# Kernel optimization log

Measured on AMD Instinct MI355X. Metric: run time of the kernel, lower is better.

## Reference

```python
import math
import jax, jax.numpy as jnp
import numpy as np

B = 8192
BAND = 5      # channels per DGCN
N = 62        # graph nodes (EEG electrodes)
LAYERS = 2
CBAM_C = (LAYERS + 1) * BAND  # 15
RED = 4
H2 = 64
K_TOP = int(N * 0.8)  # 49


def conv1x1(x, w, b):
    # x: [B,C,N,T], w: [O,C], b: [O] or None
    y = jnp.einsum('bcnt,oc->bont', x, w)
    if b is not None:
        y = y + b[None, :, None, None]
    return y


def dgcn(x, conv_w, conv_b, mem, gfc_w, gfc_b, gcn_w, gcn_b):
    skip = x
    x = conv1x1(x, conv_w, conv_b)
    scale = 1.0 / math.sqrt(BAND)
    # dynamic adjacency 1: memory-based
    a1 = jax.nn.softmax(jax.nn.relu(jnp.einsum('bcnt,cm->bnm', x, mem) * scale), axis=-1)
    # dynamic adjacency 2: self-similarity of time-summed features
    xs = jnp.sum(x, axis=-1)  # [B,C,N]
    a2 = jax.nn.softmax(jax.nn.relu(jnp.einsum('bcn,bcm->bnm', xs, xs) * scale), axis=-1)
    af = jnp.stack([a1, a2], axis=-1)          # [B,N,N,2]
    af = jnp.einsum('bnmk,ok->bnmo', af, gfc_w)[..., 0] + gfc_b[0]  # fc(2->1), squeeze
    af = jax.nn.softmax(af, axis=-1)
    _, idx = jax.lax.top_k(af, K_TOP)          # [B,N,k]
    bI = jnp.arange(af.shape[0])[:, None, None]
    nI = jnp.arange(N)[None, :, None]
    mask = jnp.zeros_like(af).at[bI, nI, idx].set(1.0)
    adj = af * mask
    # diffusion step (diffusion_step=1)
    y = jnp.einsum('bcnt,bnm->bcmt', x, adj)
    y = conv1x1(y, gcn_w, gcn_b)
    return y + skip


def cbam(x, ca_w1, ca_w2, sa_w, sa_b):
    residual = x
    # channel attention: shared SE MLP on max- and avg-pooled descriptors
    mx = jnp.max(x, axis=(2, 3), keepdims=True)   # [B,C,1,1]
    av = jnp.mean(x, axis=(2, 3), keepdims=True)
    def se(z):
        z = jnp.einsum('bcnt,oc->bont', z, ca_w1)
        z = jax.nn.relu(z)
        return jnp.einsum('bcnt,oc->bont', z, ca_w2)
    ca = jax.nn.sigmoid(se(mx) + se(av))
    out = x * ca
    # spatial attention: 3x3 conv over [max,mean] channel maps
    smax = jnp.max(out, axis=1, keepdims=True)
    smean = jnp.mean(out, axis=1, keepdims=True)
    s = jnp.concatenate([smax, smean], axis=1)    # [B,2,H,W]
    sa = jax.lax.conv_general_dilated(
        s, sa_w, window_strides=(1, 1), padding=((1, 1), (1, 1)),
        dimension_numbers=('NCHW', 'OIHW', 'NCHW')) + sa_b[None, :, None, None]
    sa = jax.nn.sigmoid(sa)
    out = out * sa
    return out + residual


def setup_inputs() -> dict:
    key = jax.random.key(0)
    ks = jax.random.split(key, 24)
    p = {}
    p['x'] = jax.random.normal(ks[0], (B, BAND * N), dtype=jnp.float32)
    for l in range(LAYERS):
        o = 1 + l * 8
        p[f'l{l}_conv_w'] = jax.random.normal(ks[o + 0], (BAND, BAND), jnp.float32) * 0.3
        p[f'l{l}_conv_b'] = jnp.zeros((BAND,), jnp.float32)
        p[f'l{l}_mem'] = jax.random.normal(ks[o + 1], (BAND, N), jnp.float32) * 0.2
        p[f'l{l}_gfc_w'] = jax.random.normal(ks[o + 2], (1, 2), jnp.float32) * 0.5
        p[f'l{l}_gfc_b'] = jnp.zeros((1,), jnp.float32)
        p[f'l{l}_gcn_w'] = jax.random.normal(ks[o + 3], (BAND, BAND), jnp.float32) * 0.3
        p[f'l{l}_gcn_b'] = jnp.zeros((BAND,), jnp.float32)
    p['ca_w1'] = jax.random.normal(ks[17], (CBAM_C // RED, CBAM_C), jnp.float32) * 0.2
    p['ca_w2'] = jax.random.normal(ks[18], (CBAM_C, CBAM_C // RED), jnp.float32) * 0.2
    p['sa_w'] = jax.random.normal(ks[19], (1, 2, 3, 3), jnp.float32) * 0.2
    p['sa_b'] = jnp.zeros((1,), jnp.float32)
    p['fc1_w'] = jax.random.normal(ks[20], (H2, N * CBAM_C), jnp.float32) * 0.03
    p['fc1_b'] = jnp.zeros((H2,), jnp.float32)
    p['fc2_w'] = jax.random.normal(ks[21], (H2, H2), jnp.float32) * 0.1
    p['fc2_b'] = jnp.zeros((H2,), jnp.float32)
    return p


def reference(x,
              l0_conv_w, l0_conv_b, l0_mem, l0_gfc_w, l0_gfc_b, l0_gcn_w, l0_gcn_b,
              l1_conv_w, l1_conv_b, l1_mem, l1_gfc_w, l1_gfc_b, l1_gcn_w, l1_gcn_b,
              ca_w1, ca_w2, sa_w, sa_b, fc1_w, fc1_b, fc2_w, fc2_b):
    h = x.reshape(x.shape[0], BAND, N)[:, :, :, None]  # [B,5,62,1]
    feats = [h]
    layer_params = [
        (l0_conv_w, l0_conv_b, l0_mem, l0_gfc_w, l0_gfc_b, l0_gcn_w, l0_gcn_b),
        (l1_conv_w, l1_conv_b, l1_mem, l1_gfc_w, l1_gfc_b, l1_gcn_w, l1_gcn_b),
    ]
    cur = h
    for lp in layer_params:
        cur = dgcn(cur, *lp)
        feats.append(cur)
    g = jnp.concatenate(feats, axis=1)                 # [B,15,62,1]
    g = cbam(g, ca_w1, ca_w2, sa_w, sa_b)
    out = g.reshape(g.shape[0], -1)
    out = jax.nn.relu(out @ fc1_w.T + fc1_b)           # dropout = identity (eval)
    out = jax.nn.relu(out @ fc2_w.T + fc2_b)
    return out
```

## Files before the change

### kernel.cpp

```cpp
#include <hip/hip_runtime.h>

#define NB 62
#define NC 5
#define KTOP 49

typedef unsigned short ushort_t;
typedef unsigned int uint_t;

__device__ __forceinline__ float sigmf(float x) {
    return 1.0f / (1.0f + __expf(-x));
}

__device__ __forceinline__ ushort_t f2b(float f) {
    union { float f; uint_t u; } cv; cv.f = f;
    uint_t r = (cv.u + 0x7fffu + ((cv.u >> 16) & 1u)) >> 16;
    return (ushort_t)r;
}
__device__ __forceinline__ float b2f(ushort_t h) {
    union { uint_t u; float f; } cv; cv.u = ((uint_t)h) << 16;
    return cv.f;
}
__device__ __forceinline__ float blo(uint_t w) {
    union { uint_t u; float f; } cv; cv.u = w << 16; return cv.f;
}
__device__ __forceinline__ float bhi(uint_t w) {
    union { uint_t u; float f; } cv; cv.u = w & 0xffff0000u; return cv.f;
}

__device__ __forceinline__ float tmax62(const float* a) {
    float t0 = a[0], t1 = a[1], t2 = a[2], t3 = a[3];
    #pragma unroll
    for (int m = 4; m < 60; m += 4) {
        t0 = fmaxf(t0, a[m]);     t1 = fmaxf(t1, a[m + 1]);
        t2 = fmaxf(t2, a[m + 2]); t3 = fmaxf(t3, a[m + 3]);
    }
    t0 = fmaxf(t0, a[60]); t1 = fmaxf(t1, a[61]);
    return fmaxf(fmaxf(t0, t1), fmaxf(t2, t3));
}
__device__ __forceinline__ float tsum62(const float* a) {
    float t0 = a[0], t1 = a[1], t2 = a[2], t3 = a[3];
    #pragma unroll
    for (int m = 4; m < 60; m += 4) {
        t0 += a[m]; t1 += a[m + 1]; t2 += a[m + 2]; t3 += a[m + 3];
    }
    t0 += a[60]; t1 += a[61];
    return (t0 + t1) + (t2 + t3);
}

__global__ void repack_kernel(const float* __restrict__ fc1w,
                              const float* __restrict__ fc2w,
                              ushort_t* __restrict__ w1o,
                              float* __restrict__ w2o) {
    const int i = blockIdx.x * 256 + threadIdx.x;
    if (i < 117 * 64 * 8) {
        const int j = i & 7, o = (i >> 3) & 63, i8 = i >> 9;
        const int src = i8 * 8 + j;
        const float v = (src < 930) ? fc1w[o * 930 + src] : 0.0f;
        w1o[i] = f2b(v);
    } else if (i < 117 * 64 * 8 + 16 * 64 * 4) {
        const int i2 = i - 117 * 64 * 8;
        const int j = i2 & 3, o = (i2 >> 2) & 63, k4 = i2 >> 8;
        w2o[i2] = fc2w[o * 64 + k4 * 4 + j];
    }
}

template <int L>
__device__ __forceinline__ void dgcn_layer(
    const int tid, const float* __restrict__ xin_g,
    const float* __restrict__ conv_w, const float* __restrict__ conv_b,
    const float* __restrict__ memp,
    const float* __restrict__ gfc_w, const float* __restrict__ gfc_b,
    const float* __restrict__ gcn_w, const float* __restrict__ gcn_b,
    float (*__restrict__ s_xc4)[4], float (*__restrict__ s_me4)[4],
    float (*__restrict__ s_t45)[2], ushort_t* __restrict__ s_adjh,
    float (*__restrict__ s_x1)[NC], float* __restrict__ f2out)
{
    const float scale = 0.44721359549995793f;

    for (int i = tid; i < NC * NB; i += 64) {
        const int c = i / NB, m = i - c * NB;
        if (c < 4) s_me4[m][c] = memp[i];
        else       s_t45[m][1] = memp[i];
    }

    float cw[25], cbv[5];
    #pragma unroll
    for (int i = 0; i < 25; ++i) cw[i] = conv_w[i];
    #pragma unroll
    for (int i = 0; i < 5; ++i)  cbv[i] = conv_b[i];
    const float w0 = gfc_w[0], w1 = gfc_w[1], b0 = gfc_b[0];

    float xo0 = 0, xo1 = 0, xo2 = 0, xo3 = 0, xo4 = 0;
    if (tid < NB) {
        float xn[5];
        #pragma unroll
        for (int c = 0; c < 5; ++c)
            xn[c] = (L == 0) ? xin_g[c * NB + tid] : s_x1[tid][c];
        xo0 = cbv[0]; xo1 = cbv[1]; xo2 = cbv[2]; xo3 = cbv[3]; xo4 = cbv[4];
        #pragma unroll
        for (int c = 0; c < 5; ++c) {
            xo0 = fmaf(cw[c],      xn[c], xo0);
            xo1 = fmaf(cw[5 + c],  xn[c], xo1);
            xo2 = fmaf(cw[10 + c], xn[c], xo2);
            xo3 = fmaf(cw[15 + c], xn[c], xo3);
            xo4 = fmaf(cw[20 + c], xn[c], xo4);
        }
        s_xc4[tid][0] = xo0; s_xc4[tid][1] = xo1;
        s_xc4[tid][2] = xo2; s_xc4[tid][3] = xo3;
        s_t45[tid][0] = xo4;
    }
    __syncthreads();

    if (tid < NB) {
        float r1[NB];
        float r2[64];
        #pragma unroll
        for (int m = 0; m < NB; ++m) {
            const float4 xc03 = *(const float4*)&s_xc4[m][0];
            const float4 me03 = *(const float4*)&s_me4[m][0];
            const float2 t45  = *(const float2*)&s_t45[m][0];
            float s1 = xo0 * me03.x + xo1 * me03.y + xo2 * me03.z + xo3 * me03.w + xo4 * t45.y;
            float s2 = xo0 * xc03.x + xo1 * xc03.y + xo2 * xc03.z + xo3 * xc03.w + xo4 * t45.x;
            r1[m] = fmaxf(s1 * scale, 0.0f);
            r2[m] = fmaxf(s2 * scale, 0.0f);
        }
        const float mx1 = tmax62(r1);
        #pragma unroll
        for (int m = 0; m < NB; ++m) r1[m] = __expf(r1[m] - mx1);
        const float inv1 = 1.0f / tsum62(r1);
        const float mx2 = tmax62(r2);
        #pragma unroll
        for (int m = 0; m < NB; ++m) r2[m] = __expf(r2[m] - mx2);
        const float inv2 = 1.0f / tsum62(r2);
        #pragma unroll
        for (int m = 0; m < NB; ++m)
            r1[m] = b0 + (r1[m] * inv1) * w0 + (r2[m] * inv2) * w1;
        const float mxa = tmax62(r1);
        #pragma unroll
        for (int m = 0; m < NB; ++m) r1[m] = __expf(r1[m] - mxa);
        const float inva = 1.0f / tsum62(r1);
        #pragma unroll
        for (int m = 0; m < NB; ++m) r1[m] *= inva;

        #pragma unroll
        for (int m = 0; m < NB; ++m) r2[m] = r1[m];
        r2[62] = INFINITY; r2[63] = INFINITY;
        #pragma unroll
        for (int k = 2; k <= 64; k <<= 1) {
            #pragma unroll
            for (int j = k >> 1; j > 0; j >>= 1) {
                #pragma unroll
                for (int i = 0; i < 64; ++i) {
                    const int p = i ^ j;
                    if (p > i) {
                        const bool up = ((i & k) == 0);
                        const float a = r2[i], c = r2[p];
                        r2[i] = up ? fminf(a, c) : fmaxf(a, c);
                        r2[p] = up ? fmaxf(a, c) : fminf(a, c);
                    }
                }
            }
        }
        const float vth = r2[13];

        int gc0 = 0, gc1 = 0, gc2 = 0, gc3 = 0;
        #pragma unroll
        for (int m = 0; m < 60; m += 4) {
            gc0 += (r1[m] > vth);     gc1 += (r1[m + 1] > vth);
            gc2 += (r1[m + 2] > vth); gc3 += (r1[m + 3] > vth);
        }
        gc0 += (r1[60] > vth); gc1 += (r1[61] > vth);
        const int G = (gc0 + gc1) + (gc2 + gc3);
        int eq = 0;
        #pragma unroll
        for (int m = 0; m < NB; ++m) {
            const bool e  = (r1[m] == vth);
            const bool ss = (r1[m] > vth) || (e && (G + eq) < KTOP);
            s_adjh[tid * NB + m] = f2b(ss ? r1[m] : 0.0f);
            eq += e ? 1 : 0;
        }
    }
    __syncthreads();

    if (tid < NB) {
        const int m = tid;
        float y0 = 0, y1 = 0, y2 = 0, y3 = 0, y4 = 0;
        for (int n = 0; n < NB; ++n) {
            const float a = b2f(s_adjh[n * NB + m]);
            const float4 xv = *(const float4*)&s_xc4[n][0];
            const float  xv4 = s_t45[n][0];
            y0 = fmaf(xv.x, a, y0); y1 = fmaf(xv.y, a, y1); y2 = fmaf(xv.z, a, y2);
            y3 = fmaf(xv.w, a, y3); y4 = fmaf(xv4, a, y4);
        }
        float gwv[25], gbv[5];
        #pragma unroll
        for (int i = 0; i < 25; ++i) gwv[i] = gcn_w[i];
        #pragma unroll
        for (int i = 0; i < 5; ++i)  gbv[i] = gcn_b[i];
        #pragma unroll
        for (int o = 0; o < 5; ++o) {
            const float z = gbv[o] + gwv[o * 5 + 0] * y0 + gwv[o * 5 + 1] * y1 +
                            gwv[o * 5 + 2] * y2 + gwv[o * 5 + 3] * y3 + gwv[o * 5 + 4] * y4;
            const float fi = (L == 0) ? xin_g[o * NB + m] : s_x1[m][o];
            const float zz = z + fi;
            if (L == 0) s_x1[m][o] = zz;
            else        f2out[o]   = zz;
        }
    }
    __syncthreads();
}

__global__ void __launch_bounds__(64) __attribute__((amdgpu_waves_per_eu(2, 3)))
encoder_kernel(
    const float* __restrict__ g_x,
    const float* __restrict__ c0w, const float* __restrict__ c0b,
    const float* __restrict__ m0,  const float* __restrict__ f0w,
    const float* __restrict__ f0b, const float* __restrict__ g0w,
    const float* __restrict__ g0b,
    const float* __restrict__ c1w, const float* __restrict__ c1b,
    const float* __restrict__ m1,  const float* __restrict__ f1w,
    const float* __restrict__ f1b, const float* __restrict__ g1w,
    const float* __restrict__ g1b,
    const float* __restrict__ caw1, const float* __restrict__ caw2,
    const float* __restrict__ saw,  const float* __restrict__ sab,
    const float* __restrict__ fc1w, const float* __restrict__ fc1b,
    const float* __restrict__ fc2w, const float* __restrict__ fc2b,
    const ushort_t* __restrict__ w1b, const float* __restrict__ w2p,
    const int use_ws,
    float* __restrict__ g_out)
{
    const int b   = blockIdx.x;
    const int tid = threadIdx.x;

    __shared__ __align__(16) float s_xc4[NB][4];
    __shared__ __align__(16) float s_me4[NB][4];
    __shared__ __align__(16) float s_t45[NB][2];
    __shared__ __align__(16) ushort_t s_adjh[NB * NB];
    __shared__ __align__(16) float s_x1[NB][NC];

    float* const s_g  = (float*)s_adjh;
    float* const s_h1 = ((float*)s_adjh) + 936;

    const float* xin = g_x + (size_t)b * (NC * NB);

    float f2[5] = {0, 0, 0, 0, 0};
    dgcn_layer<0>(tid, xin, c0w, c0b, m0, f0w, f0b, g0w, g0b,
                  s_xc4, s_me4, s_t45, s_adjh, s_x1, nullptr);
    dgcn_layer<1>(tid, xin, c1w, c1b, m1, f1w, f1b, g1w, g1b,
                  s_xc4, s_me4, s_t45, s_adjh, s_x1, f2);

    float f0[5], f1v[5];
    #pragma unroll
    for (int c = 0; c < 5; ++c) {
        f0[c]  = (tid < NB) ? xin[c * NB + tid] : 0.0f;
        f1v[c] = (tid < NB) ? s_x1[tid][c] : 0.0f;
    }

    float mxp[15], avp[15];
    #pragma unroll
    for (int c = 0; c < 15; ++c) {
        const float v = (c < 5) ? f0[c] : (c < 10) ? f1v[c - 5] : f2[c - 10];
        float vm = (tid < NB) ? v : -INFINITY;
        float vs = (tid < NB) ? v : 0.0f;
        #pragma unroll
        for (int off = 32; off > 0; off >>= 1) {
            vm = fmaxf(vm, __shfl_xor(vm, off, 64));
            vs += __shfl_xor(vs, off, 64);
        }
        mxp[c] = vm;
        avp[c] = vs * (1.0f / 62.0f);
    }
    float ca[15];
    {
        float hm[3], ha[3];
        #pragma unroll
        for (int o = 0; o < 3; ++o) {
            float am = 0.0f, aa = 0.0f;
            #pragma unroll
            for (int c = 0; c < 15; ++c) {
                const float w = caw1[o * 15 + c];
                am = fmaf(mxp[c], w, am);
                aa = fmaf(avp[c], w, aa);
            }
            hm[o] = fmaxf(am, 0.0f);
            ha[o] = fmaxf(aa, 0.0f);
        }
        #pragma unroll
        for (int c = 0; c < 15; ++c) {
            float t = 0.0f;
            #pragma unroll
            for (int o = 0; o < 3; ++o) t = fmaf(hm[o] + ha[o], caw2[c * 3 + o], t);
            ca[c] = sigmf(t);
        }
    }
    float og[15];
    float smx = -INFINITY, ssum = 0.0f;
    #pragma unroll
    for (int c = 0; c < 15; ++c) {
        const float fv = (c < 5) ? f0[c] : (c < 10) ? f1v[c - 5] : f2[c - 10];
        const float v = fv * ca[c];
        og[c] = v;
        smx = fmaxf(smx, v);
        ssum += v;
    }
    const float smean = ssum * (1.0f / 15.0f);
    const float sxl = __shfl_up(smx, 1, 64),   sml = __shfl_up(smean, 1, 64);
    const float sxr = __shfl_down(smx, 1, 64), smr = __shfl_down(smean, 1, 64);
    const float mskL = (tid > 0) ? 1.0f : 0.0f;
    const float mskR = (tid < NB - 1) ? 1.0f : 0.0f;
    float t = sab[0];
    t += mskL * (sxl * saw[1] + sml * saw[10]);
    t += smx * saw[4] + smean * saw[13];
    t += mskR * (sxr * saw[7] + smr * saw[16]);
    const float sa = sigmf(t);

    __syncthreads();
    if (tid < NB) {
        #pragma unroll
        for (int c = 0; c < 15; ++c) {
            const float fv = (c < 5) ? f0[c] : (c < 10) ? f1v[c - 5] : f2[c - 10];
            s_g[c * NB + tid] = og[c] * sa + fv;
        }
    }
    if (tid < 6) s_g[930 + tid] = 0.0f;
    __syncthreads();

    if (use_ws) {
        float acc = fc1b[tid];
        const uint4* w1v = (const uint4*)w1b;
        #pragma unroll 4
        for (int i8 = 0; i8 < 117; ++i8) {
            const uint4 wv = w1v[i8 * 64 + tid];
            const float4 ga  = *(const float4*)&s_g[i8 * 8];
            const float4 gb2 = *(const float4*)&s_g[i8 * 8 + 4];
            acc = fmaf(blo(wv.x), ga.x,  acc);
            acc = fmaf(bhi(wv.x), ga.y,  acc);
            acc = fmaf(blo(wv.y), ga.z,  acc);
            acc = fmaf(bhi(wv.y), ga.w,  acc);
            acc = fmaf(blo(wv.z), gb2.x, acc);
            acc = fmaf(bhi(wv.z), gb2.y, acc);
            acc = fmaf(blo(wv.w), gb2.z, acc);
            acc = fmaf(bhi(wv.w), gb2.w, acc);
        }
        s_h1[tid] = fmaxf(acc, 0.0f);
        __syncthreads();
        float acc2 = fc2b[tid];
        #pragma unroll
        for (int k4 = 0; k4 < 16; ++k4) {
            const float4 wv = *(const float4*)(w2p + k4 * 256 + tid * 4);
            const float4 hv = *(const float4*)&s_h1[k4 * 4];
            acc2 = fmaf(wv.x, hv.x, acc2);
            acc2 = fmaf(wv.y, hv.y, acc2);
            acc2 = fmaf(wv.z, hv.z, acc2);
            acc2 = fmaf(wv.w, hv.w, acc2);
        }
        g_out[(size_t)b * 64 + tid] = fmaxf(acc2, 0.0f);
    } else {
        float acc = fc1b[tid];
        const float* wr = fc1w + (size_t)tid * 930;
        #pragma unroll 4
        for (int i = 0; i < 928; i += 2) {
            const float2 wv = *(const float2*)(wr + i);
            const float2 gv = *(const float2*)(&s_g[i]);
            acc = fmaf(wv.x, gv.x, fmaf(wv.y, gv.y, acc));
        }
        acc += wr[928] * s_g[928] + wr[929] * s_g[929];
        s_h1[tid] = fmaxf(acc, 0.0f);
        __syncthreads();
        float acc2 = fc2b[tid];
        const float* wr2 = fc2w + tid * 64;
        #pragma unroll
        for (int k = 0; k < 64; k += 4) {
            const float4 wv = *(const float4*)(wr2 + k);
            acc2 = fmaf(wv.x, s_h1[k], acc2);
            acc2 = fmaf(wv.y, s_h1[k + 1], acc2);
            acc2 = fmaf(wv.z, s_h1[k + 2], acc2);
            acc2 = fmaf(wv.w, s_h1[k + 3], acc2);
        }
        g_out[(size_t)b * 64 + tid] = fmaxf(acc2, 0.0f);
    }
}

extern "C" void kernel_launch(void* const* d_in, const int* in_sizes, int n_in,
                              void* d_out, int out_size, void* d_ws, size_t ws_size,
                              hipStream_t stream) {
    const float* X    = (const float*)d_in[0];
    const float* C0W  = (const float*)d_in[1];
    const float* C0B  = (const float*)d_in[2];
    const float* M0   = (const float*)d_in[3];
    const float* F0W  = (const float*)d_in[4];
    const float* F0B  = (const float*)d_in[5];
    const float* G0W  = (const float*)d_in[6];
    const float* G0B  = (const float*)d_in[7];
    const float* C1W  = (const float*)d_in[8];
    const float* C1B  = (const float*)d_in[9];
    const float* M1   = (const float*)d_in[10];
    const float* F1W  = (const float*)d_in[11];
    const float* F1B  = (const float*)d_in[12];
    const float* G1W  = (const float*)d_in[13];
    const float* G1B  = (const float*)d_in[14];
    const float* CAW1 = (const float*)d_in[15];
    const float* CAW2 = (const float*)d_in[16];
    const float* SAW  = (const float*)d_in[17];
    const float* SAB  = (const float*)d_in[18];
    const float* FC1W = (const float*)d_in[19];
    const float* FC1B = (const float*)d_in[20];
    const float* FC2W = (const float*)d_in[21];
    const float* FC2B = (const float*)d_in[22];

    const int B = in_sizes[0] / (NC * NB);

    const size_t W1_BYTES = 117 * 64 * 8 * sizeof(ushort_t);
    const size_t W2_BYTES = 16 * 64 * 4 * sizeof(float);
    const int use_ws = (ws_size >= W1_BYTES + W2_BYTES) ? 1 : 0;
    ushort_t* w1b = (ushort_t*)d_ws;
    float*    w2p = (float*)((char*)d_ws + W1_BYTES);

    if (use_ws) {
        repack_kernel<<<250, 256, 0, stream>>>(FC1W, FC2W, w1b, w2p);
    }

    encoder_kernel<<<B, 64, 0, stream>>>(
        X, C0W, C0B, M0, F0W, F0B, G0W, G0B,
        C1W, C1B, M1, F1W, F1B, G1W, G1B,
        CAW1, CAW2, SAW, SAB, FC1W, FC1B, FC2W, FC2B,
        w1b, w2p, use_ws,
        (float*)d_out);
}
```

Before: 215.4 us.

## Replace 64-wide bitonic sort with chunked sort-and-merge top-14 selection

The full 64-element bitonic sort used to find the 14th-smallest threshold is replaced by sorting 16-element chunks and merging to keep only the lowest 16, which cuts compare-exchange count and register pressure. The memory matrix is now read directly from global/constant memory instead of being staged in shared memory. Adjacency is packed as bf16 pairs into 32-bit words, and the occupancy hint is raised to 4 waves per EU. Lower register use could allow more waves, but the uncached global reads of mem inside the unrolled loop may add latency.

```diff
diff --git a/kernel.cpp b/kernel.cpp
--- a/kernel.cpp
+++ b/kernel.cpp
@@ -16,15 +16,14 @@
     uint_t r = (cv.u + 0x7fffu + ((cv.u >> 16) & 1u)) >> 16;
     return (ushort_t)r;
 }
-__device__ __forceinline__ float b2f(ushort_t h) {
-    union { uint_t u; float f; } cv; cv.u = ((uint_t)h) << 16;
-    return cv.f;
-}
 __device__ __forceinline__ float blo(uint_t w) {
     union { uint_t u; float f; } cv; cv.u = w << 16; return cv.f;
 }
 __device__ __forceinline__ float bhi(uint_t w) {
     union { uint_t u; float f; } cv; cv.u = w & 0xffff0000u; return cv.f;
+}
+__device__ __forceinline__ float bits2f(uint_t u) {
+    union { uint_t u; float f; } cv; cv.u = u; return cv.f;
 }
 
 __device__ __forceinline__ float tmax62(const float* a) {
@@ -45,6 +44,44 @@
     }
     t0 += a[60]; t1 += a[61];
     return (t0 + t1) + (t2 + t3);
+}
+
+__device__ __forceinline__ void sort16(float* s) {
+    #pragma unroll
+    for (int k = 2; k <= 16; k <<= 1) {
+        #pragma unroll
+        for (int j = k >> 1; j > 0; j >>= 1) {
+            #pragma unroll
+            for (int i = 0; i < 16; ++i) {
+                const int p = i ^ j;
+                if (p > i) {
+                    const bool up = ((i & k) == 0);
+                    const float a = s[i], c = s[p];
+                    s[i] = up ? fminf(a, c) : fmaxf(a, c);
+                    s[p] = up ? fmaxf(a, c) : fminf(a, c);
+                }
+            }
+        }
+    }
+}
+__device__ __forceinline__ void merge_low16(float* m, const float* b) {
+    float t[16];
+    #pragma unroll
+    for (int i = 0; i < 16; ++i) t[i] = fminf(m[i], b[15 - i]);
+    #pragma unroll
+    for (int j = 8; j > 0; j >>= 1) {
+        #pragma unroll
+        for (int i = 0; i < 16; ++i) {
+            const int p = i ^ j;
+            if (p > i) {
+                const float a = t[i], c = t[p];
+                t[i] = fminf(a, c);
+                t[p] = fmaxf(a, c);
+            }
+        }
+    }
+    #pragma unroll
+    for (int i = 0; i < 16; ++i) m[i] = t[i];
 }
 
 __global__ void repack_kernel(const float* __restrict__ fc1w,
@@ -71,17 +108,11 @@
     const float* __restrict__ memp,
     const float* __restrict__ gfc_w, const float* __restrict__ gfc_b,
     const float* __restrict__ gcn_w, const float* __restrict__ gcn_b,
-    float (*__restrict__ s_xc4)[4], float (*__restrict__ s_me4)[4],
-    float (*__restrict__ s_t45)[2], ushort_t* __restrict__ s_adjh,
+    float (*__restrict__ s_xc4)[4], float* __restrict__ s_xc1,
+    uint_t* __restrict__ s_adj32,
     float (*__restrict__ s_x1)[NC], float* __restrict__ f2out)
 {
     const float scale = 0.44721359549995793f;
-
-    for (int i = tid; i < NC * NB; i += 64) {
-        const int c = i / NB, m = i - c * NB;
-        if (c < 4) s_me4[m][c] = memp[i];
-        else       s_t45[m][1] = memp[i];
-    }
 
     float cw[25], cbv[5];
     #pragma unroll
@@ -107,20 +138,22 @@
         }
         s_xc4[tid][0] = xo0; s_xc4[tid][1] = xo1;
         s_xc4[tid][2] = xo2; s_xc4[tid][3] = xo3;
-        s_t45[tid][0] = xo4;
+        s_xc1[tid] = xo4;
     }
     __syncthreads();
 
     if (tid < NB) {
         float r1[NB];
-        float r2[64];
+        float r2[NB];
         #pragma unroll
         for (int m = 0; m < NB; ++m) {
             const float4 xc03 = *(const float4*)&s_xc4[m][0];
-            const float4 me03 = *(const float4*)&s_me4[m][0];
-            const float2 t45  = *(const float2*)&s_t45[m][0];
-            float s1 = xo0 * me03.x + xo1 * me03.y + xo2 * me03.z + xo3 * me03.w + xo4 * t45.y;
-            float s2 = xo0 * xc03.x + xo1 * xc03.y + xo2 * xc03.z + xo3 * xc03.w + xo4 * t45.x;
+            const float  xc4  = s_xc1[m];
+            const float me0 = memp[0 * NB + m], me1 = memp[1 * NB + m];
+            const float me2 = memp[2 * NB + m], me3 = memp[3 * NB + m];
+            const float me4 = memp[4 * NB + m];
+            float s1 = xo0 * me0 + xo1 * me1 + xo2 * me2 + xo3 * me3 + xo4 * me4;
+            float s2 = xo0 * xc03.x + xo1 * xc03.y + xo2 * xc03.z + xo3 * xc03.w + xo4 * xc4;
             r1[m] = fmaxf(s1 * scale, 0.0f);
             r2[m] = fmaxf(s2 * scale, 0.0f);
         }
@@ -142,26 +175,24 @@
         #pragma unroll
         for (int m = 0; m < NB; ++m) r1[m] *= inva;
 
-        #pragma unroll
-        for (int m = 0; m < NB; ++m) r2[m] = r1[m];
-        r2[62] = INFINITY; r2[63] = INFINITY;
-        #pragma unroll
-        for (int k = 2; k <= 64; k <<= 1) {
-            #pragma unroll
-            for (int j = k >> 1; j > 0; j >>= 1) {
-                #pragma unroll
-                for (int i = 0; i < 64; ++i) {
-                    const int p = i ^ j;
-                    if (p > i) {
-                        const bool up = ((i & k) == 0);
-                        const float a = r2[i], c = r2[p];
-                        r2[i] = up ? fminf(a, c) : fmaxf(a, c);
-                        r2[p] = up ? fmaxf(a, c) : fminf(a, c);
-                    }
-                }
-            }
-        }
-        const float vth = r2[13];
+        float ga[16], gb[16];
+        #pragma unroll
+        for (int i = 0; i < 16; ++i) ga[i] = r1[i];
+        sort16(ga);
+        #pragma unroll
+        for (int i = 0; i < 16; ++i) gb[i] = r1[16 + i];
+        sort16(gb);
+        merge_low16(ga, gb);
+        #pragma unroll
+        for (int i = 0; i < 16; ++i) gb[i] = r1[32 + i];
+        sort16(gb);
+        merge_low16(ga, gb);
+        #pragma unroll
+        for (int i = 0; i < 14; ++i) gb[i] = r1[48 + i];
+        gb[14] = INFINITY; gb[15] = INFINITY;
+        sort16(gb);
+        merge_low16(ga, gb);
+        const float vth = ga[13];
 
         int gc0 = 0, gc1 = 0, gc2 = 0, gc3 = 0;
         #pragma unroll
@@ -172,11 +203,14 @@
         gc0 += (r1[60] > vth); gc1 += (r1[61] > vth);
         const int G = (gc0 + gc1) + (gc2 + gc3);
         int eq = 0;
+        uint_t pend = 0;
         #pragma unroll
         for (int m = 0; m < NB; ++m) {
             const bool e  = (r1[m] == vth);
             const bool ss = (r1[m] > vth) || (e && (G + eq) < KTOP);
-            s_adjh[tid * NB + m] = f2b(ss ? r1[m] : 0.0f);
+            const uint_t h = (uint_t)f2b(ss ? r1[m] : 0.0f);
+            if (m & 1) s_adj32[tid * 31 + (m >> 1)] = pend | (h << 16);
+            else       pend = h;
             eq += e ? 1 : 0;
         }
     }
@@ -184,11 +218,14 @@
 
     if (tid < NB) {
         const int m = tid;
+        const int dw = m >> 1;
+        const uint_t sh = (m & 1) ? 16u : 0u;
         float y0 = 0, y1 = 0, y2 = 0, y3 = 0, y4 = 0;
         for (int n = 0; n < NB; ++n) {
-            const float a = b2f(s_adjh[n * NB + m]);
+            const uint_t w = s_adj32[n * 31 + dw];
+            const float a = bits2f((w >> sh) << 16);
             const float4 xv = *(const float4*)&s_xc4[n][0];
-            const float  xv4 = s_t45[n][0];
+            const float  xv4 = s_xc1[n];
             y0 = fmaf(xv.x, a, y0); y1 = fmaf(xv.y, a, y1); y2 = fmaf(xv.z, a, y2);
             y3 = fmaf(xv.w, a, y3); y4 = fmaf(xv4, a, y4);
         }
@@ -210,7 +247,7 @@
     __syncthreads();
 }
 
-__global__ void __launch_bounds__(64) __attribute__((amdgpu_waves_per_eu(2, 3)))
+__global__ void __launch_bounds__(64) __attribute__((amdgpu_waves_per_eu(4, 4)))
 encoder_kernel(
     const float* __restrict__ g_x,
     const float* __restrict__ c0w, const float* __restrict__ c0b,
@@ -233,21 +270,20 @@
     const int tid = threadIdx.x;
 
     __shared__ __align__(16) float s_xc4[NB][4];
-    __shared__ __align__(16) float s_me4[NB][4];
-    __shared__ __align__(16) float s_t45[NB][2];
-    __shared__ __align__(16) ushort_t s_adjh[NB * NB];
+    __shared__ __align__(16) float s_xc1[NB];
+    __shared__ __align__(16) uint_t s_adj32[NB * 31];
     __shared__ __align__(16) float s_x1[NB][NC];
 
-    float* const s_g  = (float*)s_adjh;
-    float* const s_h1 = ((float*)s_adjh) + 936;
+    float* const s_g  = (float*)s_adj32;
+    float* const s_h1 = ((float*)s_adj32) + 936;
 
     const float* xin = g_x + (size_t)b * (NC * NB);
 
     float f2[5] = {0, 0, 0, 0, 0};
     dgcn_layer<0>(tid, xin, c0w, c0b, m0, f0w, f0b, g0w, g0b,
-                  s_xc4, s_me4, s_t45, s_adjh, s_x1, nullptr);
+                  s_xc4, s_xc1, s_adj32, s_x1, nullptr);
     dgcn_layer<1>(tid, xin, c1w, c1b, m1, f1w, f1b, g1w, g1b,
-                  s_xc4, s_me4, s_t45, s_adjh, s_x1, f2);
+                  s_xc4, s_xc1, s_adj32, s_x1, f2);
 
     float f0[5], f1v[5];
     #pragma unroll
@@ -331,16 +367,16 @@
         #pragma unroll 4
         for (int i8 = 0; i8 < 117; ++i8) {
             const uint4 wv = w1v[i8 * 64 + tid];
-            const float4 ga  = *(const float4*)&s_g[i8 * 8];
-            const float4 gb2 = *(const float4*)&s_g[i8 * 8 + 4];
-            acc = fmaf(blo(wv.x), ga.x,  acc);
-            acc = fmaf(bhi(wv.x), ga.y,  acc);
-            acc = fmaf(blo(wv.y), ga.z,  acc);
-            acc = fmaf(bhi(wv.y), ga.w,  acc);
-            acc = fmaf(blo(wv.z), gb2.x, acc);
-            acc = fmaf(bhi(wv.z), gb2.y, acc);
-            acc = fmaf(blo(wv.w), gb2.z, acc);
-            acc = fmaf(bhi(wv.w), gb2.w, acc);
+            const float4 ga4 = *(const float4*)&s_g[i8 * 8];
+            const float4 gb4 = *(const float4*)&s_g[i8 * 8 + 4];
+            acc = fmaf(blo(wv.x), ga4.x, acc);
+            acc = fmaf(bhi(wv.x), ga4.y, acc);
+            acc = fmaf(blo(wv.y), ga4.z, acc);
+            acc = fmaf(bhi(wv.y), ga4.w, acc);
+            acc = fmaf(blo(wv.z), gb4.x, acc);
+            acc = fmaf(bhi(wv.z), gb4.y, acc);
+            acc = fmaf(blo(wv.w), gb4.z, acc);
+            acc = fmaf(bhi(wv.w), gb4.w, acc);
         }
         s_h1[tid] = fmaxf(acc, 0.0f);
         __syncthreads();
```

Result: slower. 423.5 us (+96.6%).
